# Kernel tuning notes

Hardware: AMD Instinct MI355X
Metric: run time of the kernel (lower is better)

The kernel has to match this reference:

```python
import jax, jax.numpy as jnp
import numpy as np


def setup_inputs() -> dict:
    key = jax.random.key(0)
    ks = jax.random.split(key, 5)
    B, C, H, W = 4, 512, 64, 64
    A = 64  # attention_features
    s = lambda fan_in: 1.0 / np.sqrt(fan_in)
    return {
        "x": jax.random.normal(ks[0], (B, C, H, W), dtype=jnp.float32),
        "Wf": jax.random.normal(ks[1], (C, A), dtype=jnp.float32) * s(C),
        "bf": jnp.zeros((A,), dtype=jnp.float32),
        "Wg": jax.random.normal(ks[2], (C, A), dtype=jnp.float32) * s(C),
        "bg": jnp.zeros((A,), dtype=jnp.float32),
        "Wh": jax.random.normal(ks[3], (C, C), dtype=jnp.float32) * s(C),
        "bh": jnp.zeros((C,), dtype=jnp.float32),
        "scale": jax.random.uniform(ks[4], (), dtype=jnp.float32),
    }


def reference(x, Wf, bf, Wg, bg, Wh, bh, scale):
    B, C, H, W = x.shape
    N = H * W

    def conv1x1(w, b):  # 1x1 conv == per-pixel matmul over channels
        return jnp.einsum('bchw,cf->bfhw', x, w) + b[None, :, None, None]

    f = conv1x1(Wf, bf)  # [B, A, H, W]
    g = conv1x1(Wg, bg)  # [B, A, H, W]
    h = conv1x1(Wh, bh)  # [B, C, H, W]

    # flatten_hw (channels_first): [B, C', H, W] -> [B, N, C']
    flat = lambda t: t.reshape(B, t.shape[1], N).transpose(0, 2, 1)
    gf = flat(g)  # [B, N, A]
    ff = flat(f)  # [B, N, A]
    hf = flat(h)  # [B, N, C]

    s = jnp.einsum('bnd,bmd->bnm', gf, ff)       # [B, N, N]
    attn = jax.nn.softmax(s, axis=-1)
    o = jnp.einsum('bnm,bmc->bnc', attn, hf)     # [B, N, C]
    # Original does a raw reshape back to x's shape (no transpose) — keep it.
    y = scale * o.reshape(x.shape) + x
    return y
```

## Files before the change

### kernel.cpp

```cpp
#include <hip/hip_runtime.h>
#include <hip/hip_bf16.h>

constexpr int BB = 4;
constexpr int C  = 512;
constexpr int A  = 64;
constexpr int N  = 4096;

typedef __attribute__((ext_vector_type(8))) short s16x8;
typedef __attribute__((ext_vector_type(4))) float f32x4;

#define MFMA_16x16x32_BF16(a, b, c) __builtin_amdgcn_mfma_f32_16x16x32_bf16((a), (b), (c), 0, 0, 0)

typedef __attribute__((address_space(3))) unsigned int lds_u32_t;
typedef const __attribute__((address_space(1))) unsigned int glb_u32_t;

__device__ __forceinline__ void gl2lds16(const void* g, void* l) {
    __builtin_amdgcn_global_load_lds((glb_u32_t*)g, (lds_u32_t*)l, 16, 0, 0);
}

#define GLOAD(dst, base, off)                                                  \
    asm volatile("global_load_dwordx4 %0, %1, %2"                              \
                 : "=v"(dst) : "v"(off), "s"(base))

__global__ __launch_bounds__(256) void k_trans(const float* __restrict__ src,
                                               __hip_bfloat16* __restrict__ dst,
                                               int K, int M) {
    __shared__ __hip_bfloat16 Ls[64][66];
    int m0 = blockIdx.x << 6, k0 = blockIdx.y << 6;
    size_t bo = (size_t)blockIdx.z * K * M;
    int t = threadIdx.x;
    int lm = t & 63, g = t >> 6;
    #pragma unroll
    for (int j = 0; j < 16; ++j) {
        int kk = j * 4 + g;
        Ls[kk][lm] = __float2bfloat16(src[bo + (size_t)(k0 + kk) * M + m0 + lm]);
    }
    __syncthreads();
    #pragma unroll
    for (int j = 0; j < 16; ++j) {
        int mm = j * 4 + g;
        dst[bo + (size_t)(m0 + mm) * K + k0 + lm] = Ls[lm][mm];
    }
}

__global__ __launch_bounds__(256) void k_trans2(const float* __restrict__ src,
                                                __hip_bfloat16* __restrict__ dhi,
                                                __hip_bfloat16* __restrict__ dlo,
                                                int K, int M) {
    __shared__ float Ls[64][65];
    int m0 = blockIdx.x << 6, k0 = blockIdx.y << 6;
    size_t bo = (size_t)blockIdx.z * K * M;
    int t = threadIdx.x;
    int lm = t & 63, g = t >> 6;
    #pragma unroll
    for (int j = 0; j < 16; ++j) {
        int kk = j * 4 + g;
        Ls[kk][lm] = src[bo + (size_t)(k0 + kk) * M + m0 + lm];
    }
    __syncthreads();
    #pragma unroll
    for (int j = 0; j < 16; ++j) {
        int mm = j * 4 + g;
        float v = Ls[lm][mm];
        __hip_bfloat16 h = __float2bfloat16(v);
        size_t idx = bo + (size_t)(m0 + mm) * K + k0 + lm;
        dhi[idx] = h;
        dlo[idx] = __float2bfloat16(v - __bfloat162float(h));
    }
}

__global__ __launch_bounds__(256) void k_fgm(const __hip_bfloat16* __restrict__ XThi, const __hip_bfloat16* __restrict__ XTlo,
                                             const __hip_bfloat16* __restrict__ WfThi, const __hip_bfloat16* __restrict__ WfTlo,
                                             const __hip_bfloat16* __restrict__ WgThi, const __hip_bfloat16* __restrict__ WgTlo,
                                             const float* __restrict__ bfv, const float* __restrict__ bgv,
                                             __hip_bfloat16* __restrict__ FFhi, __hip_bfloat16* __restrict__ FFlo,
                                             __hip_bfloat16* __restrict__ GFhi, __hip_bfloat16* __restrict__ GFlo) {
    __shared__ __align__(16) __hip_bfloat16 Ah[64 * 32], Al[64 * 32];
    __shared__ __align__(16) __hip_bfloat16 Bh[128 * 32], Bl[128 * 32];
    int r0 = blockIdx.x << 6;
    int t = threadIdx.x;
    int w = t >> 6, l = t & 63;
    int ln15 = l & 15, quad = l >> 4;
    int mh = w & 1, nh = w >> 1;

    f32x4 acc[2][4];
    #pragma unroll
    for (int mi = 0; mi < 2; ++mi)
        #pragma unroll
        for (int ni = 0; ni < 4; ++ni) acc[mi][ni] = (f32x4){0.f, 0.f, 0.f, 0.f};

    for (int kt = 0; kt < C; kt += 32) {
        {
            int row = t >> 2, seg = t & 3;
            int gseg = (seg - (row >> 1)) & 3;
            size_t go = (size_t)(r0 + row) * C + kt + gseg * 8;
            gl2lds16(XThi + go, &Ah[t * 8]);
            gl2lds16(XTlo + go, &Al[t * 8]);
        }
        #pragma unroll
        for (int j = 0; j < 2; ++j) {
            int i = j * 256 + t;
            int row = i >> 2, seg = i & 3;
            int gseg = (seg - (row >> 1)) & 3;
            size_t go = (size_t)(row & 63) * C + kt + gseg * 8;
            const __hip_bfloat16* bh = j ? WgThi : WfThi;
            const __hip_bfloat16* bl = j ? WgTlo : WfTlo;
            gl2lds16(bh + go, &Bh[i * 8]);
            gl2lds16(bl + go, &Bl[i * 8]);
        }
        __syncthreads();
        s16x8 afh[2], afl[2], bfh[4], bfl[4];
        #pragma unroll
        for (int mi = 0; mi < 2; ++mi) {
            int row = mh * 32 + mi * 16 + ln15;
            int sw = ((quad + (row >> 1)) & 3) << 3;
            afh[mi] = *(const s16x8*)&Ah[row * 32 + sw];
            afl[mi] = *(const s16x8*)&Al[row * 32 + sw];
        }
        #pragma unroll
        for (int ni = 0; ni < 4; ++ni) {
            int row = nh * 64 + ni * 16 + ln15;
            int sw = ((quad + (row >> 1)) & 3) << 3;
            bfh[ni] = *(const s16x8*)&Bh[row * 32 + sw];
            bfl[ni] = *(const s16x8*)&Bl[row * 32 + sw];
        }
        #pragma unroll
        for (int mi = 0; mi < 2; ++mi)
            #pragma unroll
            for (int ni = 0; ni < 4; ++ni) {
                acc[mi][ni] = MFMA_16x16x32_BF16(afh[mi], bfh[ni], acc[mi][ni]);
                acc[mi][ni] = MFMA_16x16x32_BF16(afl[mi], bfh[ni], acc[mi][ni]);
                acc[mi][ni] = MFMA_16x16x32_BF16(afh[mi], bfl[ni], acc[mi][ni]);
            }
        __syncthreads();
    }

    #pragma unroll
    for (int mi = 0; mi < 2; ++mi) {
        #pragma unroll
        for (int r = 0; r < 4; ++r) {
            size_t grow = (size_t)(r0 + mh * 32 + mi * 16 + quad * 4 + r) * A;
            #pragma unroll
            for (int ni = 0; ni < 4; ++ni) {
                int col = nh * 64 + ni * 16 + ln15;
                if (col < A) {
                    float v = acc[mi][ni][r] + bfv[col];
                    __hip_bfloat16 h = __float2bfloat16(v);
                    FFhi[grow + col] = h;
                    FFlo[grow + col] = __float2bfloat16(v - __bfloat162float(h));
                } else {
                    int a = col - A;
                    float v = acc[mi][ni][r] + bgv[a];
                    __hip_bfloat16 h = __float2bfloat16(v);
                    GFhi[grow + a] = h;
                    GFlo[grow + a] = __float2bfloat16(v - __bfloat162float(h));
                }
            }
        }
    }
}

__global__ __launch_bounds__(256) void k_hm(const __hip_bfloat16* __restrict__ WhT,
                                            const __hip_bfloat16* __restrict__ XT,
                                            const float* __restrict__ bhv,
                                            __hip_bfloat16* __restrict__ HFT) {
    __shared__ __align__(16) __hip_bfloat16 As[128 * 32];
    __shared__ __align__(16) __hip_bfloat16 Bs[128 * 32];
    int b  = blockIdx.z;
    int c0 = blockIdx.x << 7;
    int n0 = blockIdx.y << 7;
    int t = threadIdx.x;
    int w = t >> 6, l = t & 63;
    int ln15 = l & 15, quad = l >> 4;
    int mc = (w >> 1) << 6, nn = (w & 1) << 6;

    const __hip_bfloat16* Bb = XT + (size_t)b * N * C;

    f32x4 acc[4][4];
    #pragma unroll
    for (int mi = 0; mi < 4; ++mi)
        #pragma unroll
        for (int ni = 0; ni < 4; ++ni) acc[mi][ni] = (f32x4){0.f, 0.f, 0.f, 0.f};

    for (int kt = 0; kt < C; kt += 32) {
        #pragma unroll
        for (int j = 0; j < 2; ++j) {
            int i = j * 256 + t;
            int row = i >> 2, seg = i & 3;
            int gseg = (seg - (row >> 1)) & 3;
            gl2lds16(WhT + ((size_t)(c0 + row) * C + kt + gseg * 8), &As[i * 8]);
        }
        #pragma unroll
        for (int j = 0; j < 2; ++j) {
            int i = j * 256 + t;
            int row = i >> 2, seg = i & 3;
            int gseg = (seg - (row >> 1)) & 3;
            gl2lds16(Bb + ((size_t)(n0 + row) * C + kt + gseg * 8), &Bs[i * 8]);
        }
        __syncthreads();
        s16x8 af[4], bf2[4];
        #pragma unroll
        for (int mi = 0; mi < 4; ++mi) {
            int row = mc + mi * 16 + ln15;
            int sw = ((quad + (row >> 1)) & 3) << 3;
            af[mi] = *(const s16x8*)&As[row * 32 + sw];
        }
        #pragma unroll
        for (int ni = 0; ni < 4; ++ni) {
            int row = nn + ni * 16 + ln15;
            int sw = ((quad + (row >> 1)) & 3) << 3;
            bf2[ni] = *(const s16x8*)&Bs[row * 32 + sw];
        }
        #pragma unroll
        for (int mi = 0; mi < 4; ++mi)
            #pragma unroll
            for (int ni = 0; ni < 4; ++ni)
                acc[mi][ni] = MFMA_16x16x32_BF16(af[mi], bf2[ni], acc[mi][ni]);
        __syncthreads();
    }

    #pragma unroll
    for (int mi = 0; mi < 4; ++mi) {
        #pragma unroll
        for (int r = 0; r < 4; ++r) {
            int c = c0 + mc + mi * 16 + quad * 4 + r;
            float bias = bhv[c];
            size_t rowbase = ((size_t)b * C + c) * N;
            #pragma unroll
            for (int ni = 0; ni < 4; ++ni) {
                int n = n0 + nn + ni * 16 + ln15;
                HFT[rowbase + n] = __float2bfloat16(acc[mi][ni][r] + bias);
            }
        }
    }
}

__global__ __launch_bounds__(512, 2) void k_so(const __hip_bfloat16* __restrict__ GFhi, const __hip_bfloat16* __restrict__ GFlo,
                                               const __hip_bfloat16* __restrict__ FFhi, const __hip_bfloat16* __restrict__ FFlo,
                                               const __hip_bfloat16* __restrict__ HFT,
                                               const float* __restrict__ x,
                                               const float* __restrict__ scalep,
                                               float* __restrict__ out) {
    __shared__ __align__(16) __hip_bfloat16 Hs[2][C * 64];
    __shared__ __align__(16) __hip_bfloat16 Pl[64 * 64];
    __shared__ float sred[8][32];
    __shared__ float rsum[64];

    int id  = blockIdx.x;
    int xcd = id & 7;
    int b   = xcd >> 1;
    int qs  = ((id >> 3) << 1) | (xcd & 1);
    int q0  = qs << 6;

    int t = threadIdx.x;
    int w = t >> 6, l = t & 63;
    int ln15 = l & 15, quad = l >> 4, q8 = quad << 3;
    int qh = w >> 2, kq = w & 3;
    int lr = l >> 3, ls = l & 7;

    const __hip_bfloat16* Fh = FFhi + (size_t)b * N * A;
    const __hip_bfloat16* Fl = FFlo + (size_t)b * N * A;
    const __hip_bfloat16* Hb = HFT  + (size_t)b * C * N;

    s16x8 ah[2][2], al[2][2];
    #pragma unroll
    for (int mi = 0; mi < 2; ++mi) {
        const __hip_bfloat16* gp = GFhi + (size_t)(b * N + q0 + qh * 32 + mi * 16 + ln15) * A + q8;
        const __hip_bfloat16* lp = GFlo + (size_t)(b * N + q0 + qh * 32 + mi * 16 + ln15) * A + q8;
        ah[mi][0] = *(const s16x8*)gp; ah[mi][1] = *(const s16x8*)(gp + 32);
        al[mi][0] = *(const s16x8*)lp; al[mi][1] = *(const s16x8*)(lp + 32);
    }

    f32x4 acc[4][4];
    #pragma unroll
    for (int mi = 0; mi < 4; ++mi)
        #pragma unroll
        for (int ni = 0; ni < 4; ++ni) acc[mi][ni] = (f32x4){0.f, 0.f, 0.f, 0.f};
    float sm[2][4] = {{0.f,0.f,0.f,0.f},{0.f,0.f,0.f,0.f}};

    const __hip_bfloat16* hsrc0 = Hb + (size_t)(w * 8 + lr) * N + ((ls ^ lr) << 3);
    uint32_t foff = (uint32_t)(((kq * 16 + ln15) * A + q8) * 2);
    int key2 = (kq * 16 + ln15) << 1;

#define STAGE_H(BUF, KT)                                                       \
    _Pragma("unroll")                                                          \
    for (int r = 0; r < 8; ++r)                                                \
        gl2lds16(hsrc0 + (size_t)(r * 64) * N + (KT),                          \
                 &Hs[BUF][(r * 64 + w * 8) * 64]);

    s16x8 fA[4], fB[4];
    STAGE_H(0, 0)
    GLOAD(fA[0], Fh, foff);        GLOAD(fA[1], Fh, foff + 64u);
    GLOAD(fA[2], Fl, foff);        GLOAD(fA[3], Fl, foff + 64u);

#define KITER(KT, BUF, FC, FN)                                                 \
    {                                                                          \
        int ktn = ((KT) + 64) & (N - 1);     \
        uint32_t ktnf = (uint32_t)(ktn << 7);                                  \
        STAGE_H(BUF ^ 1, ktn)                                                  \
        GLOAD(FN[0], Fh, foff + ktnf); GLOAD(FN[1], Fh, foff + ktnf + 64u);    \
        GLOAD(FN[2], Fl, foff + ktnf); GLOAD(FN[3], Fl, foff + ktnf + 64u);    \
        asm volatile("s_waitcnt vmcnt(12)" ::: "memory");                      \
        __builtin_amdgcn_sched_barrier(0);                                     \
        __builtin_amdgcn_s_setprio(1);                                         \
        _Pragma("unroll")                                                      \
        for (int mi = 0; mi < 2; ++mi) {                                       \
            f32x4 s = {0.f, 0.f, 0.f, 0.f};                                    \
            s = MFMA_16x16x32_BF16(ah[mi][0], FC[0], s);                       \
            s = MFMA_16x16x32_BF16(ah[mi][1], FC[1], s);                       \
            s = MFMA_16x16x32_BF16(al[mi][0], FC[0], s);                       \
            s = MFMA_16x16x32_BF16(al[mi][1], FC[1], s);                       \
            s = MFMA_16x16x32_BF16(ah[mi][0], FC[2], s);                       \
            s = MFMA_16x16x32_BF16(ah[mi][1], FC[3], s);                       \
            _Pragma("unroll")                                                  \
            for (int r = 0; r < 4; ++r) {                                      \
                int q = qh * 32 + mi * 16 + quad * 4 + r;                      \
                float p = __expf(s[r]);         \
                __hip_bfloat16 pb = __float2bfloat16(p);                       \
                sm[mi][r] += __bfloat162float(pb);                             \
                *(__hip_bfloat16*)((char*)Pl + q * 128 + (key2 ^ ((q & 7) << 4))) = pb; \
            }                                                                  \
        }                                                                      \
        __builtin_amdgcn_s_setprio(0);                                         \
        asm volatile("s_waitcnt lgkmcnt(0)" ::: "memory");                     \
        __builtin_amdgcn_sched_barrier(0);                                     \
        __builtin_amdgcn_s_barrier();      \
        __builtin_amdgcn_s_setprio(1);                                         \
        _Pragma("unroll")                                                      \
        for (int ks = 0; ks < 2; ++ks) {                                       \
            s16x8 pa[4], hf[4];                                                \
            _Pragma("unroll")                                                  \
            for (int mi = 0; mi < 4; ++mi) {                                   \
                int q = mi * 16 + ln15;                                        \
                pa[mi] = *(const s16x8*)((char*)Pl + q * 128 + ((ks * 64 + quad * 16) ^ ((q & 7) << 4))); \
            }                                                                  \
            _Pragma("unroll")                                                  \
            for (int ni = 0; ni < 4; ++ni) {                                   \
                int c = w * 64 + ni * 16 + ln15;                               \
                hf[ni] = *(const s16x8*)((char*)&Hs[BUF][0] + c * 128 + (((ks * 4 + quad) ^ (ln15 & 7)) << 4)); \
            }                                                                  \
            _Pragma("unroll")                                                  \
            for (int mi = 0; mi < 4; ++mi)                                     \
                _Pragma("unroll")                                              \
                for (int ni = 0; ni < 4; ++ni)                                 \
                    acc[mi][ni] = MFMA_16x16x32_BF16(pa[mi], hf[ni], acc[mi][ni]); \
        }                                                                      \
        __builtin_amdgcn_s_setprio(0);                                         \
        __builtin_amdgcn_sched_barrier(0);                                     \
        __builtin_amdgcn_s_barrier();          \
    }

    for (int kt = 0; kt < N; kt += 128) {
        KITER(kt,      0, fA, fB)
        KITER(kt + 64, 1, fB, fA)
    }
#undef KITER
#undef STAGE_H

    #pragma unroll
    for (int mi = 0; mi < 2; ++mi)
        #pragma unroll
        for (int r = 0; r < 4; ++r)
            #pragma unroll
            for (int d = 1; d < 16; d <<= 1)
                sm[mi][r] += __shfl_xor(sm[mi][r], d, 64);
    if (ln15 == 0) {
        #pragma unroll
        for (int mi = 0; mi < 2; ++mi)
            #pragma unroll
            for (int r = 0; r < 4; ++r)
                sred[w][mi * 16 + quad * 4 + r] = sm[mi][r];
    }
    __syncthreads();
    if (t < 64) {
        int base = (t >> 5) << 2, ix = t & 31;
        rsum[t] = sred[base][ix] + sred[base + 1][ix] + sred[base + 2][ix] + sred[base + 3][ix];
    }
    __syncthreads();

    float scv = *scalep;
    #pragma unroll
    for (int mi = 0; mi < 4; ++mi) {
        #pragma unroll
        for (int r = 0; r < 4; ++r) {
            int q = mi * 16 + quad * 4 + r;
            float srs = scv / rsum[q];
            size_t rowbase = (size_t)(b * N + q0 + q) * C;
            #pragma unroll
            for (int ni = 0; ni < 4; ++ni) {
                size_t idx = rowbase + w * 64 + ni * 16 + ln15;
                out[idx] = acc[mi][ni][r] * srs + x[idx];
            }
        }
    }
}

extern "C" void kernel_launch(void* const* d_in, const int* in_sizes, int n_in,
                              void* d_out, int out_size, void* d_ws, size_t ws_size,
                              hipStream_t stream) {
    const float* x   = (const float*)d_in[0];
    const float* Wf  = (const float*)d_in[1];
    const float* bfv = (const float*)d_in[2];
    const float* Wg  = (const float*)d_in[3];
    const float* bgv = (const float*)d_in[4];
    const float* Wh  = (const float*)d_in[5];
    const float* bhv = (const float*)d_in[6];
    const float* sc  = (const float*)d_in[7];
    float* out = (float*)d_out;

    char* ws = (char*)d_ws;
    size_t off = 0;
    __hip_bfloat16* FFhi = (__hip_bfloat16*)(ws + off); off += (size_t)BB * N * A * 2;
    __hip_bfloat16* FFlo = (__hip_bfloat16*)(ws + off); off += (size_t)BB * N * A * 2;
    __hip_bfloat16* GFhi = (__hip_bfloat16*)(ws + off); off += (size_t)BB * N * A * 2;
    __hip_bfloat16* GFlo = (__hip_bfloat16*)(ws + off); off += (size_t)BB * N * A * 2;
    __hip_bfloat16* HFT  = (__hip_bfloat16*)(ws + off); off += (size_t)BB * C * N * 2;
    char* Pbase          = (ws + off);                  off += (size_t)BB * N * N * 2;
    off += (size_t)BB * N * 4;
    __hip_bfloat16* WhT  = (__hip_bfloat16*)(ws + off); off += (size_t)C * C * 2;
    __hip_bfloat16* WfThi = (__hip_bfloat16*)(ws + off); off += (size_t)A * C * 2;
    __hip_bfloat16* WfTlo = (__hip_bfloat16*)(ws + off); off += (size_t)A * C * 2;
    __hip_bfloat16* WgThi = (__hip_bfloat16*)(ws + off); off += (size_t)A * C * 2;
    __hip_bfloat16* WgTlo = (__hip_bfloat16*)(ws + off); off += (size_t)A * C * 2;
    __hip_bfloat16* XThi = (__hip_bfloat16*)(Pbase + (size_t)BB * N * N * 2 - (size_t)BB * N * C * 2);
    __hip_bfloat16* XTlo = (__hip_bfloat16*)(Pbase + (size_t)BB * N * N * 2 - 2 * (size_t)BB * N * C * 2);

    k_trans<<<dim3(C / 64, C / 64, 1), dim3(256), 0, stream>>>(Wh, WhT, C, C);
    k_trans2<<<dim3(N / 64, C / 64, BB), dim3(256), 0, stream>>>(x, XThi, XTlo, C, N);
    k_trans2<<<dim3(A / 64, C / 64, 1), dim3(256), 0, stream>>>(Wf, WfThi, WfTlo, C, A);
    k_trans2<<<dim3(A / 64, C / 64, 1), dim3(256), 0, stream>>>(Wg, WgThi, WgTlo, C, A);
    k_hm<<<dim3(C / 128, N / 128, BB), dim3(256), 0, stream>>>(WhT, XThi, bhv, HFT);
    k_fgm<<<dim3((BB * N) / 64), dim3(256), 0, stream>>>(XThi, XTlo, WfThi, WfTlo, WgThi, WgTlo,
                                                         bfv, bgv, FFhi, FFlo, GFhi, GFlo);
    k_so<<<dim3(BB * (N / 64)), dim3(512), 0, stream>>>(GFhi, GFlo, FFhi, FFlo, HFT, x, sc, out);
}
```

Baseline: 284.1 us.

## Split attention-output kernel across channel halves with smaller 256-thread blocks

Each k_so block now computes only 256 of the 512 output channels, doubling the grid and halving block size and the H staging buffer in LDS. Each wave computes scores for 32 keys instead of 16, and memory wait counts are retuned for the larger F prefetch. The goal is to shrink LDS per block and improve occupancy and scheduling. The cost is that the QK^T scores and exponentials are computed twice per query tile, once per channel half.

```diff
diff --git a/kernel.cpp b/kernel.cpp
--- a/kernel.cpp
+++ b/kernel.cpp
@@ -235,32 +235,33 @@
     }
 }
 
-__global__ __launch_bounds__(512, 2) void k_so(const __hip_bfloat16* __restrict__ GFhi, const __hip_bfloat16* __restrict__ GFlo,
+__global__ __launch_bounds__(256, 2) void k_so(const __hip_bfloat16* __restrict__ GFhi, const __hip_bfloat16* __restrict__ GFlo,
                                                const __hip_bfloat16* __restrict__ FFhi, const __hip_bfloat16* __restrict__ FFlo,
                                                const __hip_bfloat16* __restrict__ HFT,
                                                const float* __restrict__ x,
                                                const float* __restrict__ scalep,
                                                float* __restrict__ out) {
-    __shared__ __align__(16) __hip_bfloat16 Hs[2][C * 64];
+    __shared__ __align__(16) __hip_bfloat16 Hs[2][256 * 64];
     __shared__ __align__(16) __hip_bfloat16 Pl[64 * 64];
-    __shared__ float sred[8][32];
+    __shared__ float sred[4][32];
     __shared__ float rsum[64];
 
     int id  = blockIdx.x;
     int xcd = id & 7;
     int b   = xcd >> 1;
-    int qs  = ((id >> 3) << 1) | (xcd & 1);
+    int cb  = xcd & 1;
+    int qs  = id >> 3;
     int q0  = qs << 6;
 
     int t = threadIdx.x;
     int w = t >> 6, l = t & 63;
     int ln15 = l & 15, quad = l >> 4, q8 = quad << 3;
-    int qh = w >> 2, kq = w & 3;
+    int qh = w >> 1, kq = w & 1;
     int lr = l >> 3, ls = l & 7;
 
     const __hip_bfloat16* Fh = FFhi + (size_t)b * N * A;
     const __hip_bfloat16* Fl = FFlo + (size_t)b * N * A;
-    const __hip_bfloat16* Hb = HFT  + (size_t)b * C * N;
+    const __hip_bfloat16* Hb = HFT + ((size_t)b * C + cb * 256) * N;
 
     s16x8 ah[2][2], al[2][2];
     #pragma unroll
@@ -279,52 +280,61 @@
     float sm[2][4] = {{0.f,0.f,0.f,0.f},{0.f,0.f,0.f,0.f}};
 
     const __hip_bfloat16* hsrc0 = Hb + (size_t)(w * 8 + lr) * N + ((ls ^ lr) << 3);
-    uint32_t foff = (uint32_t)(((kq * 16 + ln15) * A + q8) * 2);
-    int key2 = (kq * 16 + ln15) << 1;
+    uint32_t foffk[2];
+    foffk[0] = (uint32_t)(((kq * 32 + ln15) * A + q8) * 2);
+    foffk[1] = (uint32_t)(((kq * 32 + 16 + ln15) * A + q8) * 2);
 
 #define STAGE_H(BUF, KT)                                                       \
     _Pragma("unroll")                                                          \
     for (int r = 0; r < 8; ++r)                                                \
-        gl2lds16(hsrc0 + (size_t)(r * 64) * N + (KT),                          \
-                 &Hs[BUF][(r * 64 + w * 8) * 64]);
-
-    s16x8 fA[4], fB[4];
+        gl2lds16(hsrc0 + (size_t)(r * 32) * N + (KT),                          \
+                 &Hs[BUF][(r * 32 + w * 8) * 64]);
+
+#define LOAD_F(FN, KTNF)                                                       \
+    GLOAD(FN[0], Fh, foffk[0] + (KTNF)); GLOAD(FN[1], Fh, foffk[0] + (KTNF) + 64u); \
+    GLOAD(FN[2], Fl, foffk[0] + (KTNF)); GLOAD(FN[3], Fl, foffk[0] + (KTNF) + 64u); \
+    GLOAD(FN[4], Fh, foffk[1] + (KTNF)); GLOAD(FN[5], Fh, foffk[1] + (KTNF) + 64u); \
+    GLOAD(FN[6], Fl, foffk[1] + (KTNF)); GLOAD(FN[7], Fl, foffk[1] + (KTNF) + 64u);
+
+    s16x8 fA[8], fB[8];
+    LOAD_F(fA, 0u)
     STAGE_H(0, 0)
-    GLOAD(fA[0], Fh, foff);        GLOAD(fA[1], Fh, foff + 64u);
-    GLOAD(fA[2], Fl, foff);        GLOAD(fA[3], Fl, foff + 64u);
 
 #define KITER(KT, BUF, FC, FN)                                                 \
     {                                                                          \
         int ktn = ((KT) + 64) & (N - 1);     \
         uint32_t ktnf = (uint32_t)(ktn << 7);                                  \
+        LOAD_F(FN, ktnf)                                                       \
         STAGE_H(BUF ^ 1, ktn)                                                  \
-        GLOAD(FN[0], Fh, foff + ktnf); GLOAD(FN[1], Fh, foff + ktnf + 64u);    \
-        GLOAD(FN[2], Fl, foff + ktnf); GLOAD(FN[3], Fl, foff + ktnf + 64u);    \
-        asm volatile("s_waitcnt vmcnt(12)" ::: "memory");                      \
+        asm volatile("s_waitcnt vmcnt(24)" ::: "memory");                      \
         __builtin_amdgcn_sched_barrier(0);                                     \
         __builtin_amdgcn_s_setprio(1);                                         \
         _Pragma("unroll")                                                      \
-        for (int mi = 0; mi < 2; ++mi) {                                       \
-            f32x4 s = {0.f, 0.f, 0.f, 0.f};                                    \
-            s = MFMA_16x16x32_BF16(ah[mi][0], FC[0], s);                       \
-            s = MFMA_16x16x32_BF16(ah[mi][1], FC[1], s);                       \
-            s = MFMA_16x16x32_BF16(al[mi][0], FC[0], s);                       \
-            s = MFMA_16x16x32_BF16(al[mi][1], FC[1], s);                       \
-            s = MFMA_16x16x32_BF16(ah[mi][0], FC[2], s);                       \
-            s = MFMA_16x16x32_BF16(ah[mi][1], FC[3], s);                       \
+        for (int mi = 0; mi < 2; ++mi)                                         \
             _Pragma("unroll")                                                  \
-            for (int r = 0; r < 4; ++r) {                                      \
-                int q = qh * 32 + mi * 16 + quad * 4 + r;                      \
-                float p = __expf(s[r]);         \
-                __hip_bfloat16 pb = __float2bfloat16(p);                       \
-                sm[mi][r] += __bfloat162float(pb);                             \
-                *(__hip_bfloat16*)((char*)Pl + q * 128 + (key2 ^ ((q & 7) << 4))) = pb; \
+            for (int kk = 0; kk < 2; ++kk) {                                   \
+                f32x4 s = {0.f, 0.f, 0.f, 0.f};                                \
+                s = MFMA_16x16x32_BF16(ah[mi][0], FC[kk * 4 + 0], s);          \
+                s = MFMA_16x16x32_BF16(ah[mi][1], FC[kk * 4 + 1], s);          \
+                s = MFMA_16x16x32_BF16(al[mi][0], FC[kk * 4 + 0], s);          \
+                s = MFMA_16x16x32_BF16(al[mi][1], FC[kk * 4 + 1], s);          \
+                s = MFMA_16x16x32_BF16(ah[mi][0], FC[kk * 4 + 2], s);          \
+                s = MFMA_16x16x32_BF16(ah[mi][1], FC[kk * 4 + 3], s);          \
+                int key2 = (kq * 32 + kk * 16 + ln15) << 1;                    \
+                _Pragma("unroll")                                              \
+                for (int r = 0; r < 4; ++r) {                                  \
+                    int q = qh * 32 + mi * 16 + quad * 4 + r;                  \
+                    float p = __expf(s[r]);     \
+                    __hip_bfloat16 pb = __float2bfloat16(p);                   \
+                    sm[mi][r] += __bfloat162float(pb);                         \
+                    *(__hip_bfloat16*)((char*)Pl + q * 128 + (key2 ^ ((q & 7) << 4))) = pb; \
+                }                                                              \
             }                                                                  \
-        }                                                                      \
         __builtin_amdgcn_s_setprio(0);                                         \
         asm volatile("s_waitcnt lgkmcnt(0)" ::: "memory");                     \
+        asm volatile("s_waitcnt vmcnt(16)" ::: "memory");                      \
         __builtin_amdgcn_sched_barrier(0);                                     \
-        __builtin_amdgcn_s_barrier();      \
+        __builtin_amdgcn_s_barrier();            \
         __builtin_amdgcn_s_setprio(1);                                         \
         _Pragma("unroll")                                                      \
         for (int ks = 0; ks < 2; ++ks) {                                       \
@@ -337,7 +347,7 @@
             _Pragma("unroll")                                                  \
             for (int ni = 0; ni < 4; ++ni) {                                   \
                 int c = w * 64 + ni * 16 + ln15;                               \
-                hf[ni] = *(const s16x8*)((char*)&Hs[BUF][0] + c * 128 + (((ks * 4 + quad) ^ (ln15 & 7)) << 4)); \
+                hf[ni] = *(const s16x8*)((char*)&Hs[BUF][0] + c * 128 + ((ks * 64 + quad * 16) ^ ((c & 7) << 4))); \
             }                                                                  \
             _Pragma("unroll")                                                  \
             for (int mi = 0; mi < 4; ++mi)                                     \
@@ -356,6 +366,7 @@
     }
 #undef KITER
 #undef STAGE_H
+#undef LOAD_F
 
     #pragma unroll
     for (int mi = 0; mi < 2; ++mi)
@@ -373,8 +384,8 @@
     }
     __syncthreads();
     if (t < 64) {
-        int base = (t >> 5) << 2, ix = t & 31;
-        rsum[t] = sred[base][ix] + sred[base + 1][ix] + sred[base + 2][ix] + sred[base + 3][ix];
+        int hq = t >> 5, row = t & 31;
+        rsum[t] = sred[hq * 2][row] + sred[hq * 2 + 1][row];
     }
     __syncthreads();
 
@@ -385,7 +396,7 @@
         for (int r = 0; r < 4; ++r) {
             int q = mi * 16 + quad * 4 + r;
             float srs = scv / rsum[q];
-            size_t rowbase = (size_t)(b * N + q0 + q) * C;
+            size_t rowbase = (size_t)(b * N + q0 + q) * C + cb * 256;
             #pragma unroll
             for (int ni = 0; ni < 4; ++ni) {
                 size_t idx = rowbase + w * 64 + ni * 16 + ln15;
@@ -432,5 +443,5 @@
     k_hm<<<dim3(C / 128, N / 128, BB), dim3(256), 0, stream>>>(WhT, XThi, bhv, HFT);
     k_fgm<<<dim3((BB * N) / 64), dim3(256), 0, stream>>>(XThi, XTlo, WfThi, WfTlo, WgThi, WgTlo,
                                                          bfv, bgv, FFhi, FFlo, GFhi, GFlo);
-    k_so<<<dim3(BB * (N / 64)), dim3(512), 0, stream>>>(GFhi, GFlo, FFhi, FFlo, HFT, x, sc, out);
-}
+    k_so<<<dim3(BB * (N / 64) * 2), dim3(256), 0, stream>>>(GFhi, GFlo, FFhi, FFlo, HFT, x, sc, out);
+}
```

Result: slower. 322.0 us (+13.4%).

## Software-pipeline QK and PV stages with double-buffered P tile

Applied to the files above, without the earlier changes.

Double-buffers the probability tile in LDS so the QK/exp step for the next key tile runs in the same phase as the PV MFMA step for the current tile. This removes one of the two block barriers per key tile. The change adds a prologue, an epilogue and a deeper prefetch of the F operands, so F loads are issued two tiles ahead. It costs 8KB more LDS and more live registers, which could hurt the occupancy of 2 blocks per CU.

```diff
diff --git a/kernel.cpp b/kernel.cpp
--- a/kernel.cpp
+++ b/kernel.cpp
@@ -242,7 +242,7 @@
                                                const float* __restrict__ scalep,
                                                float* __restrict__ out) {
     __shared__ __align__(16) __hip_bfloat16 Hs[2][C * 64];
-    __shared__ __align__(16) __hip_bfloat16 Pl[64 * 64];
+    __shared__ __align__(16) __hip_bfloat16 Pl[2][64 * 64];
     __shared__ float sred[8][32];
     __shared__ float rsum[64];
 
@@ -288,73 +288,96 @@
         gl2lds16(hsrc0 + (size_t)(r * 64) * N + (KT),                          \
                  &Hs[BUF][(r * 64 + w * 8) * 64]);
 
-    s16x8 fA[4], fB[4];
-    STAGE_H(0, 0)
-    GLOAD(fA[0], Fh, foff);        GLOAD(fA[1], Fh, foff + 64u);
-    GLOAD(fA[2], Fl, foff);        GLOAD(fA[3], Fl, foff + 64u);
-
-#define KITER(KT, BUF, FC, FN)                                                 \
+#define LOAD_F(FN, KTF)                                                        \
+    GLOAD(FN[0], Fh, foff + (KTF));      GLOAD(FN[1], Fh, foff + (KTF) + 64u); \
+    GLOAD(FN[2], Fl, foff + (KTF));      GLOAD(FN[3], Fl, foff + (KTF) + 64u);
+
+#define QK_STEP(PW, FC)                                                        \
+    _Pragma("unroll")                                                          \
+    for (int mi = 0; mi < 2; ++mi) {                                           \
+        f32x4 s = {0.f, 0.f, 0.f, 0.f};                                        \
+        s = MFMA_16x16x32_BF16(ah[mi][0], FC[0], s);                           \
+        s = MFMA_16x16x32_BF16(ah[mi][1], FC[1], s);                           \
+        s = MFMA_16x16x32_BF16(al[mi][0], FC[0], s);                           \
+        s = MFMA_16x16x32_BF16(al[mi][1], FC[1], s);                           \
+        s = MFMA_16x16x32_BF16(ah[mi][0], FC[2], s);                           \
+        s = MFMA_16x16x32_BF16(ah[mi][1], FC[3], s);                           \
+        _Pragma("unroll")                                                      \
+        for (int r = 0; r < 4; ++r) {                                          \
+            int q = qh * 32 + mi * 16 + quad * 4 + r;                          \
+            float p = __expf(s[r]);             \
+            __hip_bfloat16 pb = __float2bfloat16(p);                           \
+            sm[mi][r] += __bfloat162float(pb);                                 \
+            *(__hip_bfloat16*)((char*)&Pl[PW][0] + q * 128 + (key2 ^ ((q & 7) << 4))) = pb; \
+        }                                                                      \
+    }
+
+#define PV_STEP(PR, HR)                                                        \
+    _Pragma("unroll")                                                          \
+    for (int ks = 0; ks < 2; ++ks) {                                           \
+        s16x8 pa[4], hf[4];                                                    \
+        _Pragma("unroll")                                                      \
+        for (int mi = 0; mi < 4; ++mi) {                                       \
+            int q = mi * 16 + ln15;                                            \
+            pa[mi] = *(const s16x8*)((char*)&Pl[PR][0] + q * 128 + ((ks * 64 + quad * 16) ^ ((q & 7) << 4))); \
+        }                                                                      \
+        _Pragma("unroll")                                                      \
+        for (int ni = 0; ni < 4; ++ni) {                                       \
+            int c = w * 64 + ni * 16 + ln15;                                   \
+            hf[ni] = *(const s16x8*)((char*)&Hs[HR][0] + c * 128 + (((ks * 4 + quad) ^ (ln15 & 7)) << 4)); \
+        }                                                                      \
+        _Pragma("unroll")                                                      \
+        for (int mi = 0; mi < 4; ++mi)                                         \
+            _Pragma("unroll")                                                  \
+            for (int ni = 0; ni < 4; ++ni)                                     \
+                acc[mi][ni] = MFMA_16x16x32_BF16(pa[mi], hf[ni], acc[mi][ni]); \
+    }
+
+#define KBODY(KT, HW, HR, PW, PR, FC, FN)                                      \
     {                                                                          \
-        int ktn = ((KT) + 64) & (N - 1);     \
-        uint32_t ktnf = (uint32_t)(ktn << 7);                                  \
-        STAGE_H(BUF ^ 1, ktn)                                                  \
-        GLOAD(FN[0], Fh, foff + ktnf); GLOAD(FN[1], Fh, foff + ktnf + 64u);    \
-        GLOAD(FN[2], Fl, foff + ktnf); GLOAD(FN[3], Fl, foff + ktnf + 64u);    \
-        asm volatile("s_waitcnt vmcnt(12)" ::: "memory");                      \
+        int ktn1 = (KT) + 64;                                                  \
+        int ktn2 = ((KT) + 128) & (N - 1);        \
+        STAGE_H(HW, ktn1)                                                      \
+        LOAD_F(FN, (uint32_t)(ktn2 << 7))                                      \
+        asm volatile("s_waitcnt vmcnt(12)" ::: "memory");    \
         __builtin_amdgcn_sched_barrier(0);                                     \
         __builtin_amdgcn_s_setprio(1);                                         \
-        _Pragma("unroll")                                                      \
-        for (int mi = 0; mi < 2; ++mi) {                                       \
-            f32x4 s = {0.f, 0.f, 0.f, 0.f};                                    \
-            s = MFMA_16x16x32_BF16(ah[mi][0], FC[0], s);                       \
-            s = MFMA_16x16x32_BF16(ah[mi][1], FC[1], s);                       \
-            s = MFMA_16x16x32_BF16(al[mi][0], FC[0], s);                       \
-            s = MFMA_16x16x32_BF16(al[mi][1], FC[1], s);                       \
-            s = MFMA_16x16x32_BF16(ah[mi][0], FC[2], s);                       \
-            s = MFMA_16x16x32_BF16(ah[mi][1], FC[3], s);                       \
-            _Pragma("unroll")                                                  \
-            for (int r = 0; r < 4; ++r) {                                      \
-                int q = qh * 32 + mi * 16 + quad * 4 + r;                      \
-                float p = __expf(s[r]);         \
-                __hip_bfloat16 pb = __float2bfloat16(p);                       \
-                sm[mi][r] += __bfloat162float(pb);                             \
-                *(__hip_bfloat16*)((char*)Pl + q * 128 + (key2 ^ ((q & 7) << 4))) = pb; \
-            }                                                                  \
-        }                                                                      \
+        QK_STEP(PW, FC)                                                        \
+        PV_STEP(PR, HR)                                                        \
         __builtin_amdgcn_s_setprio(0);                                         \
-        asm volatile("s_waitcnt lgkmcnt(0)" ::: "memory");                     \
+        asm volatile("s_waitcnt vmcnt(4)" ::: "memory");    \
+        asm volatile("s_waitcnt lgkmcnt(0)" ::: "memory");  \
         __builtin_amdgcn_sched_barrier(0);                                     \
-        __builtin_amdgcn_s_barrier();      \
-        __builtin_amdgcn_s_setprio(1);                                         \
-        _Pragma("unroll")                                                      \
-        for (int ks = 0; ks < 2; ++ks) {                                       \
-            s16x8 pa[4], hf[4];                                                \
-            _Pragma("unroll")                                                  \
-            for (int mi = 0; mi < 4; ++mi) {                                   \
-                int q = mi * 16 + ln15;                                        \
-                pa[mi] = *(const s16x8*)((char*)Pl + q * 128 + ((ks * 64 + quad * 16) ^ ((q & 7) << 4))); \
-            }                                                                  \
-            _Pragma("unroll")                                                  \
-            for (int ni = 0; ni < 4; ++ni) {                                   \
-                int c = w * 64 + ni * 16 + ln15;                               \
-                hf[ni] = *(const s16x8*)((char*)&Hs[BUF][0] + c * 128 + (((ks * 4 + quad) ^ (ln15 & 7)) << 4)); \
-            }                                                                  \
-            _Pragma("unroll")                                                  \
-            for (int mi = 0; mi < 4; ++mi)                                     \
-                _Pragma("unroll")                                              \
-                for (int ni = 0; ni < 4; ++ni)                                 \
-                    acc[mi][ni] = MFMA_16x16x32_BF16(pa[mi], hf[ni], acc[mi][ni]); \
-        }                                                                      \
-        __builtin_amdgcn_s_setprio(0);                                         \
-        __builtin_amdgcn_sched_barrier(0);                                     \
-        __builtin_amdgcn_s_barrier();          \
-    }
-
-    for (int kt = 0; kt < N; kt += 128) {
-        KITER(kt,      0, fA, fB)
-        KITER(kt + 64, 1, fB, fA)
-    }
-#undef KITER
+        __builtin_amdgcn_s_barrier();                                          \
+    }
+
+    s16x8 fA[4], fB[4];
+    LOAD_F(fA, 0u)
+    STAGE_H(0, 0)
+    LOAD_F(fB, (uint32_t)(64 << 7))
+    asm volatile("s_waitcnt vmcnt(12)" ::: "memory");
+    __builtin_amdgcn_sched_barrier(0);
+    QK_STEP(0, fA)
+    asm volatile("s_waitcnt vmcnt(4)" ::: "memory");
+    asm volatile("s_waitcnt lgkmcnt(0)" ::: "memory");
+    __builtin_amdgcn_sched_barrier(0);
+    __builtin_amdgcn_s_barrier();
+
+    int kt = 0;
+    for (int it = 0; it < 31; ++it) {
+        KBODY(kt,      1, 0, 1, 0, fB, fA)
+        KBODY(kt + 64, 0, 1, 0, 1, fA, fB)
+        kt += 128;
+    }
+    KBODY(kt, 1, 0, 1, 0, fB, fA)
+    __builtin_amdgcn_s_setprio(1);
+    PV_STEP(1, 1)
+    __builtin_amdgcn_s_setprio(0);
+
+#undef KBODY
+#undef PV_STEP
+#undef QK_STEP
+#undef LOAD_F
 #undef STAGE_H
 
     #pragma unroll
```

New measurement: 281.7 us. No clear change (-0.8%).
